# Kernel optimization log

Measured on AMD Instinct MI355X. Metric: run time of the kernel, lower is better.

Reference implementation:

```python
import jax, jax.numpy as jnp
import numpy as np
import math

B, T, D, H, L = 64, 255, 512, 8, 8
CODEBOOK = 512
V = CODEBOOK + 3  # bos/eos/pad
COND_DIM = 512
MAX_LEN = 256
HD = D // H


def _layernorm(x, g, b, eps=1e-5):
    mu = jnp.mean(x, axis=-1, keepdims=True)
    var = jnp.mean(jnp.square(x - mu), axis=-1, keepdims=True)
    return (x - mu) * jax.lax.rsqrt(var + eps) * g + b


def setup_inputs() -> dict:
    key = jax.random.key(0)
    ks = jax.random.split(key, 24)
    s = 0.02
    d = {
        'tokens': jax.random.randint(ks[0], (B, T), 0, V),
        'cond': jax.random.normal(ks[1], (B, COND_DIM), jnp.float32),
        'emb': jax.random.normal(ks[2], (V, D), jnp.float32) * s,  # tied token_emb / head weight
        'pos_emb': jax.random.normal(ks[3], (1, MAX_LEN, D), jnp.float32) * s,
        'cond_w1': jax.random.normal(ks[4], (COND_DIM, D), jnp.float32) * s,
        'cond_b1': jnp.zeros((D,), jnp.float32),
        'cond_w2': jax.random.normal(ks[5], (D, D), jnp.float32) * s,
        'cond_b2': jnp.zeros((D,), jnp.float32),
        'ln1_g': jnp.ones((L, D), jnp.float32),
        'ln1_b': jnp.zeros((L, D), jnp.float32),
        'qkv_w': jax.random.normal(ks[6], (L, D, 3 * D), jnp.float32) * s,
        'qkv_b': jnp.zeros((L, 3 * D), jnp.float32),
        'proj_w': jax.random.normal(ks[7], (L, D, D), jnp.float32) * s,
        'proj_b': jnp.zeros((L, D), jnp.float32),
        'ln2_g': jnp.ones((L, D), jnp.float32),
        'ln2_b': jnp.zeros((L, D), jnp.float32),
        'mlp_w1': jax.random.normal(ks[8], (L, D, 4 * D), jnp.float32) * s,
        'mlp_b1': jnp.zeros((L, 4 * D), jnp.float32),
        'mlp_w2': jax.random.normal(ks[9], (L, 4 * D, D), jnp.float32) * s,
        'mlp_b2': jnp.zeros((L, D), jnp.float32),
        'lnf_g': jnp.ones((D,), jnp.float32),
        'lnf_b': jnp.zeros((D,), jnp.float32),
    }
    return d


def reference(tokens, cond, emb, pos_emb, cond_w1, cond_b1, cond_w2, cond_b2,
              ln1_g, ln1_b, qkv_w, qkv_b, proj_w, proj_b,
              ln2_g, ln2_b, mlp_w1, mlp_b1, mlp_w2, mlp_b2, lnf_g, lnf_b):
    b, t = tokens.shape
    h = emb[tokens] + pos_emb[:, :t, :]                              # [B,T,D]
    c = jax.nn.silu(cond @ cond_w1 + cond_b1) @ cond_w2 + cond_b2    # [B,D]
    h = jnp.concatenate([c[:, None, :], h], axis=1)                  # [B,S,D]
    S = t + 1
    causal = jnp.tril(jnp.ones((S, S), bool))
    scale = 1.0 / math.sqrt(HD)
    for i in range(L):
        x = _layernorm(h, ln1_g[i], ln1_b[i])
        qkv = (x @ qkv_w[i] + qkv_b[i]).reshape(b, S, 3, H, HD).transpose(2, 0, 3, 1, 4)
        q, k, v = qkv[0], qkv[1], qkv[2]                             # [B,H,S,hd]
        a = jnp.einsum('bhsd,bhtd->bhst', q, k) * scale
        a = jnp.where(causal, a, -jnp.inf)
        a = jax.nn.softmax(a, axis=-1)
        o = jnp.einsum('bhst,bhtd->bhsd', a, v).transpose(0, 2, 1, 3).reshape(b, S, D)
        h = h + o @ proj_w[i] + proj_b[i]
        x = _layernorm(h, ln2_g[i], ln2_b[i])
        h = h + jax.nn.gelu(x @ mlp_w1[i] + mlp_b1[i], approximate=False) @ mlp_w2[i] + mlp_b2[i]
    h = _layernorm(h, lnf_g, lnf_b)
    return (h @ emb.T)[:, 1:, :]                                     # [B,T,V]
```

## Files before the change

kernel.cpp:

```cpp
#include <hip/hip_runtime.h>
#include <hip/hip_bf16.h>

typedef __attribute__((ext_vector_type(8))) short bf16x8;
typedef __attribute__((ext_vector_type(4))) float f32x4;
typedef __attribute__((ext_vector_type(2))) unsigned short u16x2;
typedef __attribute__((ext_vector_type(4))) unsigned short u16x4;
typedef __attribute__((ext_vector_type(8))) unsigned short u16x8;
typedef unsigned short u16;

#define DEV static __device__ __forceinline__

DEV float bf2f(u16 u) {
  union { unsigned int i; float f; } c; c.i = ((unsigned int)u) << 16; return c.f;
}
DEV u16 f2bf(float f) {
  union { float f; unsigned int i; } c; c.f = f;
  unsigned int i = c.i;
  i += 0x7FFFu + ((i >> 16) & 1u);
  return (u16)(i >> 16);
}

DEV void gload_lds16(const void* g, void* l) {
  __builtin_amdgcn_global_load_lds((const __attribute__((address_space(1))) void*)g,
                                   (__attribute__((address_space(3))) void*)l, 16, 0, 0);
}

DEV f32x4 mfma16(bf16x8 a, bf16x8 b, f32x4 c) {
  return __builtin_amdgcn_mfma_f32_16x16x32_bf16(a, b, c, 0, 0, 0);
}

template<int N> DEV void vwait() { asm volatile("s_waitcnt vmcnt(%0)" :: "n"(N) : "memory"); }

DEV float gelu(float x) {
  float t2 = __builtin_fmaf(0.044715f * x * x, x, x);
  float e = __expf(1.5957691216f * t2);
  float th = 1.f - 2.f / (e + 1.f);
  return 0.5f * x * (1.f + th);
}

__global__ __launch_bounds__(256) void ktranspose(const float* __restrict__ in, u16* __restrict__ out,
                                                  int K, int N) {
  __shared__ u16 tile[32][33];
  const float* src = in + (size_t)blockIdx.z * K * N;
  u16* dst = out + (size_t)blockIdx.z * K * N;
  const int n0 = blockIdx.x * 32, k0 = blockIdx.y * 32;
  const int tx = threadIdx.x, ty = threadIdx.y;
#pragma unroll
  for (int i = ty; i < 32; i += 8) tile[i][tx] = f2bf(src[(size_t)(k0 + i) * N + n0 + tx]);
  __syncthreads();
#pragma unroll
  for (int i = ty; i < 32; i += 8) dst[(size_t)(n0 + i) * K + k0 + tx] = tile[tx][i];
}

__global__ __launch_bounds__(256) void kcvt(const float* __restrict__ in, u16* __restrict__ out, int n) {
  int i = blockIdx.x * 256 + threadIdx.x;
  if (i < n) out[i] = f2bf(in[i]);
}

__global__ __launch_bounds__(256) void kcond(const float* __restrict__ cond, const float* __restrict__ w1,
                                             const float* __restrict__ b1, const float* __restrict__ w2,
                                             const float* __restrict__ b2, u16* __restrict__ h) {
  __shared__ float xr[512];
  __shared__ float t1[512];
  const int b = blockIdx.x, tid = threadIdx.x;
  for (int i = tid; i < 512; i += 256) xr[i] = cond[b * 512 + i];
  __syncthreads();
  for (int j = tid; j < 512; j += 256) {
    float acc = b1[j];
    for (int k = 0; k < 512; ++k) acc += xr[k] * w1[k * 512 + j];
    t1[j] = acc / (1.f + __expf(-acc));
  }
  __syncthreads();
  for (int j = tid; j < 512; j += 256) {
    float acc = b2[j];
    for (int k = 0; k < 512; ++k) acc += t1[k] * w2[k * 512 + j];
    h[(size_t)b * 256 * 512 + j] = f2bf(acc);
  }
}

__global__ __launch_bounds__(256) void kembed(const int* __restrict__ tok, const float* __restrict__ emb,
                                              const float* __restrict__ pos, u16* __restrict__ h) {
  const int idx = blockIdx.x;
  const int b = idx / 255, t = idx % 255;
  const int c = threadIdx.x * 2;
  const int tk = tok[idx];
  float2 ev = *(const float2*)(emb + (size_t)tk * 512 + c);
  float2 pv = *(const float2*)(pos + (size_t)t * 512 + c);
  u16x2 r;
  r[0] = f2bf(ev.x + pv.x);
  r[1] = f2bf(ev.y + pv.y);
  *(u16x2*)(h + ((size_t)b * 256 + 1 + t) * 512 + c) = r;
}

__global__ __launch_bounds__(256) void kln(const u16* __restrict__ hin, const float* __restrict__ g,
                                           const float* __restrict__ bt, u16* __restrict__ out) {
  const int row = blockIdx.x * 4 + (threadIdx.x >> 6), lane = threadIdx.x & 63;
  u16x8 xv = *(const u16x8*)(hin + (size_t)row * 512 + lane * 8);
  float x[8];
  float s1 = 0.f, s2 = 0.f;
#pragma unroll
  for (int j = 0; j < 8; ++j) {
    x[j] = bf2f(xv[j]);
    s1 += x[j];
    s2 += x[j] * x[j];
  }
#pragma unroll
  for (int off = 1; off < 64; off <<= 1) { s1 += __shfl_xor(s1, off); s2 += __shfl_xor(s2, off); }
  float mu = s1 * (1.f / 512.f);
  float var = s2 * (1.f / 512.f) - mu * mu;
  float rs = rsqrtf(var + 1e-5f);
  const int c0 = lane * 8;
  float4 g0 = *(const float4*)(g + c0), g1 = *(const float4*)(g + c0 + 4);
  float4 b0 = *(const float4*)(bt + c0), b1 = *(const float4*)(bt + c0 + 4);
  u16x8 o;
  o[0] = f2bf((x[0] - mu) * rs * g0.x + b0.x);
  o[1] = f2bf((x[1] - mu) * rs * g0.y + b0.y);
  o[2] = f2bf((x[2] - mu) * rs * g0.z + b0.z);
  o[3] = f2bf((x[3] - mu) * rs * g0.w + b0.w);
  o[4] = f2bf((x[4] - mu) * rs * g1.x + b1.x);
  o[5] = f2bf((x[5] - mu) * rs * g1.y + b1.y);
  o[6] = f2bf((x[6] - mu) * rs * g1.z + b1.z);
  o[7] = f2bf((x[7] - mu) * rs * g1.w + b1.w);
  *(u16x8*)(out + (size_t)row * 512 + c0) = o;
}

template<int MODE>
__global__ __launch_bounds__(256, 2) void kgemm3(const u16* __restrict__ A, const u16* __restrict__ Bt,
                                                 const float* __restrict__ bias, void* __restrict__ Cout,
                                                 int M, int N, int K) {
  __shared__ __align__(16) u16 As[3][4096];
  __shared__ __align__(16) u16 Bs[3][4096];
  const int tid = threadIdx.x;
  const int lane = tid & 63;
  const int wr = tid >> 7, wc = (tid >> 6) & 1;
  const int m0 = blockIdx.x * 128, n0 = blockIdx.y * 128;
  const int nkt = K >> 5;
  const size_t Kb = (size_t)K * 2;

  const int srow = tid >> 2;
  const int schunk = tid & 3;
  const int sc = schunk ^ ((srow >> 1) & 3);
  const int d1 = tid * 16, d2 = tid * 16 + 4096;
  int brA = n0 + srow, brB = n0 + srow + 64;
  if (MODE == 3) { brA = min(brA, N - 1); brB = min(brB, N - 1); }
  const char* Ab = (const char*)A;
  const char* Bb = (const char*)Bt;
  const size_t a0 = (size_t)(m0 + srow) * Kb + sc * 16;
  const size_t a1 = (size_t)(m0 + srow + 64) * Kb + sc * 16;
  const size_t b0 = (size_t)brA * Kb + sc * 16;
  const size_t b1 = (size_t)brB * Kb + sc * 16;

  f32x4 acc[4][4];
#pragma unroll
  for (int i = 0; i < 4; ++i)
#pragma unroll
    for (int j = 0; j < 4; ++j) acc[i][j] = f32x4{0.f, 0.f, 0.f, 0.f};

#pragma unroll
  for (int t = 0; t < 2; ++t) {
    const size_t ko = (size_t)t * 64;
    gload_lds16(Ab + a0 + ko, (char*)As[t] + d1);
    gload_lds16(Ab + a1 + ko, (char*)As[t] + d2);
    gload_lds16(Bb + b0 + ko, (char*)Bs[t] + d1);
    gload_lds16(Bb + b1 + ko, (char*)Bs[t] + d2);
  }
  asm volatile("s_waitcnt vmcnt(4)" ::: "memory");
  __builtin_amdgcn_s_barrier();
  __builtin_amdgcn_sched_barrier(0);

  const int kchunk = (((lane >> 4) ^ ((lane >> 1) & 3)) << 4);
  const int arow = wr * 64 + (lane & 15);
  const int brow = wc * 64 + (lane & 15);

  for (int kt = 0; kt < nkt; ++kt) {
    const int bufc = kt % 3;
    const bool deep = (kt + 2 < nkt);
    if (deep) {
      const int bufn = (kt + 2) % 3;
      const size_t ko = (size_t)(kt + 2) * 64;
      gload_lds16(Ab + a0 + ko, (char*)As[bufn] + d1);
      gload_lds16(Ab + a1 + ko, (char*)As[bufn] + d2);
      gload_lds16(Bb + b0 + ko, (char*)Bs[bufn] + d1);
      gload_lds16(Bb + b1 + ko, (char*)Bs[bufn] + d2);
    }
    const char* Ap = (const char*)As[bufc];
    const char* Bp = (const char*)Bs[bufc];
    bf16x8 aF[4], bF[4];
#pragma unroll
    for (int mt = 0; mt < 4; ++mt) aF[mt] = *(const bf16x8*)(Ap + (arow + mt * 16) * 64 + kchunk);
#pragma unroll
    for (int nt = 0; nt < 4; ++nt) bF[nt] = *(const bf16x8*)(Bp + (brow + nt * 16) * 64 + kchunk);
#pragma unroll
    for (int mt = 0; mt < 4; ++mt)
#pragma unroll
      for (int nt = 0; nt < 4; ++nt)
        acc[mt][nt] = mfma16(aF[mt], bF[nt], acc[mt][nt]);
    if (deep) {
      asm volatile("s_waitcnt vmcnt(4)" ::: "memory");
    } else {
      asm volatile("s_waitcnt vmcnt(0)" ::: "memory");
    }
    __builtin_amdgcn_s_barrier();
    __builtin_amdgcn_sched_barrier(0);
  }

  float bv[4];
#pragma unroll
  for (int nt = 0; nt < 4; ++nt) {
    int col = n0 + wc * 64 + nt * 16 + (lane & 15);
    bv[nt] = (MODE == 3) ? 0.f : bias[col];
  }

  if (MODE == 0 || MODE == 1) {
    u16* C = (u16*)Cout;
#pragma unroll
    for (int mt = 0; mt < 4; ++mt)
#pragma unroll
      for (int r = 0; r < 4; ++r) {
        int row = m0 + wr * 64 + mt * 16 + (lane >> 4) * 4 + r;
        u16* cp = C + (size_t)row * N + n0 + wc * 64 + (lane & 15);
#pragma unroll
        for (int nt = 0; nt < 4; ++nt) {
          float v = acc[mt][nt][r] + bv[nt];
          if (MODE == 1) v = gelu(v);
          cp[nt * 16] = f2bf(v);
        }
      }
  } else {
    float* C = (float*)Cout;
#pragma unroll
    for (int mt = 0; mt < 4; ++mt)
#pragma unroll
      for (int r = 0; r < 4; ++r) {
        int row = m0 + wr * 64 + mt * 16 + (lane >> 4) * 4 + r;
        int s = row & 255;
        if (s == 0) continue;
        int bb = row >> 8;
        float* cp = C + ((size_t)bb * 255 + (s - 1)) * 515 + n0 + wc * 64 + (lane & 15);
#pragma unroll
        for (int nt = 0; nt < 4; ++nt) {
          int col = n0 + wc * 64 + nt * 16 + (lane & 15);
          if (col < 515) cp[nt * 16] = acc[mt][nt][r];
        }
      }
  }
}

template<int FM>
__global__ __launch_bounds__(512, 2) void kgemm8(const u16* __restrict__ A, const u16* __restrict__ Bt,
                                                 const float* __restrict__ bias, u16* __restrict__ h,
                                                 int M, int N, int K) {
  constexpr int ABYTES = FM * 32 * 128;
  constexpr int BBYTES = 256 * 128;
  constexpr int AH = ABYTES / 2, BH = BBYTES / 2;
  constexpr int ALD = AH / 8192;
  constexpr int BOFF = 2 * ABYTES;
  constexpr int BM = FM * 32;
  __shared__ __align__(16) char shm[2 * ABYTES + 2 * BBYTES];

  const int tid = threadIdx.x;
  const int lane = tid & 63;
  const int wid = tid >> 6;
  const int wr = wid >> 2;
  const int wc = wid & 3;
  const int fr = lane & 15, fq = lane >> 4;
  const int axor = (fr & 7) << 4;
  const int m0 = blockIdx.x * BM, n0 = blockIdx.y * 256;
  const int nkt = K >> 6;
  const int Kb = K * 2;
  const char* Ab = (const char*)A;
  const char* Bb = (const char*)Bt;

  unsigned aOff[2][ALD], bOff[2][2];
#pragma unroll
  for (int hh = 0; hh < 2; ++hh) {
#pragma unroll
    for (int j = 0; j < ALD; ++j) {
      int d = hh * AH + j * 8192 + tid * 16;
      int row = d >> 7, pc = (d >> 4) & 7;
      aOff[hh][j] = (unsigned)((m0 + row) * Kb + ((pc ^ (row & 7)) << 4));
    }
#pragma unroll
    for (int j = 0; j < 2; ++j) {
      int d = hh * BH + j * 8192 + tid * 16;
      int row = d >> 7, pc = (d >> 4) & 7;
      bOff[hh][j] = (unsigned)((n0 + row) * Kb + ((pc ^ (row & 7)) << 4));
    }
  }

  auto stA = [&](int kt, int hh, int b) {
#pragma unroll
    for (int j = 0; j < ALD; ++j)
      gload_lds16(Ab + (size_t)aOff[hh][j] + (size_t)kt * 128,
                  shm + b * ABYTES + hh * AH + j * 8192 + tid * 16);
  };
  auto stB = [&](int kt, int hh, int b) {
#pragma unroll
    for (int j = 0; j < 2; ++j)
      gload_lds16(Bb + (size_t)bOff[hh][j] + (size_t)kt * 128,
                  shm + BOFF + b * BBYTES + hh * BH + j * 8192 + tid * 16);
  };
  auto rdA = [&](int b, int m, int ks) {
    return *(const bf16x8*)(shm + b * ABYTES + (wr * (BM / 2) + m * 16 + fr) * 128 +
                            ((ks * 64 + fq * 16) ^ axor));
  };
  auto rdB = [&](int b, int n, int ks) {
    return *(const bf16x8*)(shm + BOFF + b * BBYTES + (wc * 64 + n * 16 + fr) * 128 +
                            ((ks * 64 + fq * 16) ^ axor));
  };

  f32x4 acc[FM][4];
#pragma unroll
  for (int i = 0; i < FM; ++i)
#pragma unroll
    for (int j = 0; j < 4; ++j) acc[i][j] = f32x4{0.f, 0.f, 0.f, 0.f};

  stA(0, 0, 0); stA(0, 1, 0); stB(0, 0, 0); stB(0, 1, 0);
  if (nkt > 1) { stA(1, 0, 1); stA(1, 1, 1); }
  vwait<2 * ALD>();
  __builtin_amdgcn_sched_barrier(0);
  __builtin_amdgcn_s_barrier();

  for (int kt = 0; kt < nkt; ++kt) {
    const int cur = kt & 1;
    const bool sb = (kt + 1 < nkt);
    const bool sa = (kt + 2 < nkt);
    bf16x8 aF[FM][2], bF[4][2];
#pragma unroll
    for (int m = 0; m < FM; ++m) aF[m][0] = rdA(cur, m, 0);
#pragma unroll
    for (int n = 0; n < 4; ++n) bF[n][0] = rdB(cur, n, 0);
    if (sb) stB(kt + 1, 0, cur ^ 1);
    __builtin_amdgcn_s_barrier();
    __builtin_amdgcn_s_setprio(1);
#pragma unroll
    for (int m = 0; m < FM / 2; ++m)
#pragma unroll
      for (int n = 0; n < 4; ++n) acc[m][n] = mfma16(aF[m][0], bF[n][0], acc[m][n]);
    __builtin_amdgcn_s_setprio(0);
    __builtin_amdgcn_s_barrier();
#pragma unroll
    for (int m = 0; m < FM; ++m) aF[m][1] = rdA(cur, m, 1);
#pragma unroll
    for (int n = 0; n < 4; ++n) bF[n][1] = rdB(cur, n, 1);
    if (sb) stB(kt + 1, 1, cur ^ 1);
    __builtin_amdgcn_s_barrier();
    __builtin_amdgcn_s_setprio(1);
#pragma unroll
    for (int m = FM / 2; m < FM; ++m)
#pragma unroll
      for (int n = 0; n < 4; ++n) acc[m][n] = mfma16(aF[m][0], bF[n][0], acc[m][n]);
    __builtin_amdgcn_s_setprio(0);
    asm volatile("s_waitcnt lgkmcnt(0)" ::: "memory");
    __builtin_amdgcn_sched_barrier(0);
    __builtin_amdgcn_s_barrier();
    if (sa) stA(kt + 2, 0, cur);
    __builtin_amdgcn_s_barrier();
    __builtin_amdgcn_s_setprio(1);
#pragma unroll
    for (int m = 0; m < FM / 2; ++m)
#pragma unroll
      for (int n = 0; n < 4; ++n) acc[m][n] = mfma16(aF[m][1], bF[n][1], acc[m][n]);
    __builtin_amdgcn_s_setprio(0);
    __builtin_amdgcn_s_barrier();
    if (sa) stA(kt + 2, 1, cur);
    __builtin_amdgcn_s_barrier();
    __builtin_amdgcn_s_setprio(1);
#pragma unroll
    for (int m = FM / 2; m < FM; ++m)
#pragma unroll
      for (int n = 0; n < 4; ++n) acc[m][n] = mfma16(aF[m][1], bF[n][1], acc[m][n]);
    __builtin_amdgcn_s_setprio(0);
    if (sa) vwait<2 * ALD>(); else vwait<0>();
    __builtin_amdgcn_sched_barrier(0);
    __builtin_amdgcn_s_barrier();
  }

  float bv[4];
#pragma unroll
  for (int n = 0; n < 4; ++n) bv[n] = bias[n0 + wc * 64 + n * 16 + fr];

#pragma unroll
  for (int m = 0; m < FM; ++m)
#pragma unroll
    for (int r = 0; r < 4; ++r) {
      int row = m0 + wr * (BM / 2) + m * 16 + fq * 4 + r;
      u16* hp = h + (size_t)row * N + n0 + wc * 64 + fr;
#pragma unroll
      for (int n = 0; n < 4; ++n) {
        float val = acc[m][n][r] + bv[n] + bf2f(hp[n * 16]);
        hp[n * 16] = f2bf(val);
      }
    }
}

__global__ __launch_bounds__(256, 1) void kattn(const u16* __restrict__ qkv, u16* __restrict__ o) {
  __shared__ __align__(16) u16 Ks[256][72];
  __shared__ __align__(16) u16 Vt[64][264];
  __shared__ __align__(16) u16 Ps[4][64][72];
  const int tid = threadIdx.x, wv = tid >> 6, lane = tid & 63;
  const int bh = blockIdx.x, bb = bh >> 3, hh = bh & 7;
  const size_t base = (size_t)bb * 256 * 1536 + hh * 64;

  for (int c = tid; c < 2048; c += 256) {
    int s = c >> 3, pp = c & 7;
    u16x8 kv = *(const u16x8*)(qkv + base + (size_t)s * 1536 + 512 + pp * 8);
    *(u16x8*)&Ks[s][pp * 8] = kv;
    u16x8 vv = *(const u16x8*)(qkv + base + (size_t)s * 1536 + 1024 + pp * 8);
#pragma unroll
    for (int j = 0; j < 8; ++j) Vt[pp * 8 + j][s] = vv[j];
  }
  __syncthreads();

  bf16x8 qf[4][2];
#pragma unroll
  for (int mt = 0; mt < 4; ++mt)
#pragma unroll
    for (int ks = 0; ks < 2; ++ks)
      qf[mt][ks] = *(const bf16x8*)(qkv + base +
                   (size_t)(wv * 64 + mt * 16 + (lane & 15)) * 1536 + ks * 32 + (lane >> 4) * 8);

  const float scale = 0.125f;
  float mrow[4][4], lsum[4][4];
#pragma unroll
  for (int mt = 0; mt < 4; ++mt)
#pragma unroll
    for (int r = 0; r < 4; ++r) { mrow[mt][r] = -1e30f; lsum[mt][r] = 0.f; }

  f32x4 oacc[4][4];
#pragma unroll
  for (int i = 0; i < 4; ++i)
#pragma unroll
    for (int j = 0; j < 4; ++j) oacc[i][j] = f32x4{0.f, 0.f, 0.f, 0.f};

  for (int ct = 0; ct <= wv; ++ct) {
    f32x4 sacc[4][4];
#pragma unroll
    for (int i = 0; i < 4; ++i)
#pragma unroll
      for (int j = 0; j < 4; ++j) sacc[i][j] = f32x4{0.f, 0.f, 0.f, 0.f};
#pragma unroll
    for (int ks = 0; ks < 2; ++ks) {
      bf16x8 kf[4];
#pragma unroll
      for (int nt = 0; nt < 4; ++nt)
        kf[nt] = *(const bf16x8*)&Ks[ct * 64 + nt * 16 + (lane & 15)][ks * 32 + (lane >> 4) * 8];
#pragma unroll
      for (int mt = 0; mt < 4; ++mt)
#pragma unroll
        for (int nt = 0; nt < 4; ++nt)
          sacc[mt][nt] = mfma16(qf[mt][ks], kf[nt], sacc[mt][nt]);
    }
#pragma unroll
    for (int mt = 0; mt < 4; ++mt)
#pragma unroll
      for (int r = 0; r < 4; ++r) {
        int srow = wv * 64 + mt * 16 + (lane >> 4) * 4 + r;
        float v[4];
        float mx = -1e30f;
#pragma unroll
        for (int nt = 0; nt < 4; ++nt) {
          int tcol = ct * 64 + nt * 16 + (lane & 15);
          float vv = sacc[mt][nt][r] * scale;
          v[nt] = (tcol > srow) ? -1e30f : vv;
          mx = fmaxf(mx, v[nt]);
        }
#pragma unroll
        for (int off = 1; off < 16; off <<= 1) mx = fmaxf(mx, __shfl_xor(mx, off));
        float mnew = fmaxf(mrow[mt][r], mx);
        float sf = __expf(mrow[mt][r] - mnew);
        mrow[mt][r] = mnew;
        float ps = 0.f;
#pragma unroll
        for (int nt = 0; nt < 4; ++nt) {
          float pe = (v[nt] <= -1e29f) ? 0.f : __expf(v[nt] - mnew);
          ps += pe;
          Ps[wv][mt * 16 + (lane >> 4) * 4 + r][nt * 16 + (lane & 15)] = f2bf(pe);
        }
#pragma unroll
        for (int off = 1; off < 16; off <<= 1) ps += __shfl_xor(ps, off);
        lsum[mt][r] = lsum[mt][r] * sf + ps;
#pragma unroll
        for (int nt = 0; nt < 4; ++nt) oacc[mt][nt][r] *= sf;
      }
#pragma unroll
    for (int ks = 0; ks < 2; ++ks) {
      bf16x8 pf[4], vf[4];
#pragma unroll
      for (int mt = 0; mt < 4; ++mt)
        pf[mt] = *(const bf16x8*)&Ps[wv][mt * 16 + (lane & 15)][ks * 32 + (lane >> 4) * 8];
#pragma unroll
      for (int nt = 0; nt < 4; ++nt)
        vf[nt] = *(const bf16x8*)&Vt[nt * 16 + (lane & 15)][ct * 64 + ks * 32 + (lane >> 4) * 8];
#pragma unroll
      for (int mt = 0; mt < 4; ++mt)
#pragma unroll
        for (int nt = 0; nt < 4; ++nt)
          oacc[mt][nt] = mfma16(pf[mt], vf[nt], oacc[mt][nt]);
    }
  }

#pragma unroll
  for (int mt = 0; mt < 4; ++mt)
#pragma unroll
    for (int r = 0; r < 4; ++r) {
      int s = wv * 64 + mt * 16 + (lane >> 4) * 4 + r;
      float inv = 1.f / lsum[mt][r];
      u16* op = o + ((size_t)bb * 256 + s) * 512 + hh * 64 + (lane & 15);
#pragma unroll
      for (int nt = 0; nt < 4; ++nt) op[nt * 16] = f2bf(oacc[mt][nt][r] * inv);
    }
}

extern "C" void kernel_launch(void* const* d_in, const int* in_sizes, int n_in,
                              void* d_out, int out_size, void* d_ws, size_t ws_size,
                              hipStream_t stream) {
  const int* tokens = (const int*)d_in[0];
  const float* cond = (const float*)d_in[1];
  const float* emb = (const float*)d_in[2];
  const float* pos = (const float*)d_in[3];
  const float* cw1 = (const float*)d_in[4];
  const float* cb1 = (const float*)d_in[5];
  const float* cw2 = (const float*)d_in[6];
  const float* cb2 = (const float*)d_in[7];
  const float* ln1g = (const float*)d_in[8];
  const float* ln1b = (const float*)d_in[9];
  const float* qkvw = (const float*)d_in[10];
  const float* qkvb = (const float*)d_in[11];
  const float* projw = (const float*)d_in[12];
  const float* projb = (const float*)d_in[13];
  const float* ln2g = (const float*)d_in[14];
  const float* ln2b = (const float*)d_in[15];
  const float* w1 = (const float*)d_in[16];
  const float* b1 = (const float*)d_in[17];
  const float* w2 = (const float*)d_in[18];
  const float* b2 = (const float*)d_in[19];
  const float* lnfg = (const float*)d_in[20];
  const float* lnfb = (const float*)d_in[21];

  const size_t NEEDED = (size_t)16384 * 512 * 2
                      + (size_t)16384 * 512 * 2
                      + (size_t)16384 * 2048 * 2
                      + (size_t)8 * 1536 * 512 * 2
                      + (size_t)8 * 512 * 512 * 2
                      + (size_t)8 * 2048 * 512 * 2
                      + (size_t)8 * 512 * 2048 * 2;
  if (ws_size < NEEDED) return;

  char* p = (char*)d_ws;
  u16* h = (u16*)p;            p += (size_t)16384 * 512 * 2;
  u16* xln = (u16*)p;          p += (size_t)16384 * 512 * 2;
  u16* big = (u16*)p;          p += (size_t)16384 * 2048 * 2;
  u16* attn_o = big + (size_t)16384 * 1536;
  u16* embB = big;
  u16* qkvT = (u16*)p;         p += (size_t)8 * 1536 * 512 * 2;
  u16* projT = (u16*)p;        p += (size_t)8 * 512 * 512 * 2;
  u16* w1T = (u16*)p;          p += (size_t)8 * 2048 * 512 * 2;
  u16* w2T = (u16*)p;          p += (size_t)8 * 512 * 2048 * 2;

  ktranspose<<<dim3(48, 16, 8), dim3(32, 8), 0, stream>>>(qkvw, qkvT, 512, 1536);
  ktranspose<<<dim3(16, 16, 8), dim3(32, 8), 0, stream>>>(projw, projT, 512, 512);
  ktranspose<<<dim3(64, 16, 8), dim3(32, 8), 0, stream>>>(w1, w1T, 512, 2048);
  ktranspose<<<dim3(16, 64, 8), dim3(32, 8), 0, stream>>>(w2, w2T, 2048, 512);

  kembed<<<16320, 256, 0, stream>>>(tokens, emb, pos, h);
  kcond<<<64, 256, 0, stream>>>(cond, cw1, cb1, cw2, cb2, h);

  for (int l = 0; l < 8; ++l) {
    kln<<<4096, 256, 0, stream>>>(h, ln1g + l * 512, ln1b + l * 512, xln);
    kgemm3<0><<<dim3(128, 12), 256, 0, stream>>>(xln, qkvT + (size_t)l * 1536 * 512,
                                                 qkvb + l * 1536, big, 16384, 1536, 512);
    kattn<<<512, 256, 0, stream>>>(big, attn_o);
    kgemm8<4><<<dim3(128, 2), 512, 0, stream>>>(attn_o, projT + (size_t)l * 512 * 512,
                                                projb + l * 512, h, 16384, 512, 512);
    kln<<<4096, 256, 0, stream>>>(h, ln2g + l * 512, ln2b + l * 512, xln);
    kgemm3<1><<<dim3(128, 16), 256, 0, stream>>>(xln, w1T + (size_t)l * 2048 * 512,
                                                 b1 + l * 2048, big, 16384, 2048, 512);
    kgemm8<4><<<dim3(128, 2), 512, 0, stream>>>(big, w2T + (size_t)l * 512 * 2048,
                                                b2 + l * 512, h, 16384, 512, 2048);
  }
  kln<<<4096, 256, 0, stream>>>(h, lnfg, lnfb, xln);
  kcvt<<<1030, 256, 0, stream>>>(emb, embB, 515 * 512);
  kgemm3<3><<<dim3(128, 5), 256, 0, stream>>>(xln, embB, nullptr, d_out, 16384, 515, 512);
}
```

Baseline: 1.878 ms.

## Keep full-K weight panel resident in LDS for QKV and MLP-up GEMMs

Adds a GEMM kernel that loads a 128xK weight panel into shared memory once per block and streams eight 128-row A tiles through a triple-buffered pipeline. The bias and GELU epilogue is written out after each M tile. QKV and MLP-up projections switch to it. This avoids reloading the weight tile for every M tile, but it uses about 128 KB of LDS for one block per CU, a much smaller grid, and serialised epilogues inside the main loop.

```diff
diff --git a/kernel.cpp b/kernel.cpp
--- a/kernel.cpp
+++ b/kernel.cpp
@@ -124,6 +124,106 @@
   *(u16x8*)(out + (size_t)row * 512 + c0) = o;
 }
 
+template<int MODE, int MT>
+__global__ __launch_bounds__(256, 1) void kgemmbs(const u16* __restrict__ A, const u16* __restrict__ Bt,
+                                                  const float* __restrict__ bias, u16* __restrict__ C,
+                                                  int M, int N, int K) {
+  __shared__ __align__(16) u16 Bp[128 * 512];
+  __shared__ __align__(16) u16 As[3][4096];
+  const int tid = threadIdx.x, lane = tid & 63;
+  const int wr = tid >> 7, wc = (tid >> 6) & 1;
+  const int fr = lane & 15, fq = lane >> 4;
+  const int n0 = blockIdx.y * 128;
+  const int m0 = blockIdx.x * (MT * 128);
+  const int NKT = 16;
+  const size_t Kb = (size_t)K * 2;
+  const char* Ab = (const char*)A;
+  const char* Bb = (const char*)Bt;
+
+#pragma unroll
+  for (int j = 0; j < 32; ++j) {
+    int d = tid * 16 + j * 4096;
+    int row = d >> 10, off = d & 1023;
+    gload_lds16(Bb + (size_t)(n0 + row) * Kb + (off ^ ((row & 7) << 4)), (char*)Bp + d);
+  }
+
+  const int srow = tid >> 2;
+  const int sc = (tid & 3) ^ ((srow >> 1) & 3);
+  const int d1 = tid * 16, d2 = tid * 16 + 4096;
+  auto stageA = [&](int g, int buf) {
+    const int mt = g >> 4, kt = g & 15;
+    const size_t base = (size_t)(m0 + mt * 128 + srow) * Kb + kt * 64 + sc * 16;
+    gload_lds16(Ab + base, (char*)As[buf] + d1);
+    gload_lds16(Ab + base + (size_t)64 * Kb, (char*)As[buf] + d2);
+  };
+
+  stageA(0, 0);
+  stageA(1, 1);
+  asm volatile("s_waitcnt vmcnt(2)" ::: "memory");
+  __builtin_amdgcn_s_barrier();
+  __builtin_amdgcn_sched_barrier(0);
+
+  const int kchunkA = (((lane >> 4) ^ ((lane >> 1) & 3)) << 4);
+  const int arow = wr * 64 + fr;
+  const int brow0 = wc * 64 + fr;
+
+  f32x4 acc[4][4];
+#pragma unroll
+  for (int i = 0; i < 4; ++i)
+#pragma unroll
+    for (int j = 0; j < 4; ++j) acc[i][j] = f32x4{0.f, 0.f, 0.f, 0.f};
+
+  float bv[4], dummy = 0.f;
+#pragma unroll
+  for (int nt = 0; nt < 4; ++nt) bv[nt] = bias[n0 + wc * 64 + nt * 16 + fr];
+
+  const int TOT = MT * NKT;
+  for (int g = 0; g < TOT; ++g) {
+    const int kt = g & 15;
+    const int bufc = g % 3;
+    if (g + 2 < TOT) stageA(g + 2, (g + 2) % 3);
+    const char* Ap = (const char*)As[bufc];
+    bf16x8 aF[4], bF[4];
+#pragma unroll
+    for (int mt4 = 0; mt4 < 4; ++mt4)
+      aF[mt4] = *(const bf16x8*)(Ap + (arow + mt4 * 16) * 64 + kchunkA);
+#pragma unroll
+    for (int nt = 0; nt < 4; ++nt) {
+      const int nrow = brow0 + nt * 16;
+      const int koff = (kt * 64 + fq * 16) ^ ((nrow & 7) << 4);
+      bF[nt] = *(const bf16x8*)((const char*)Bp + nrow * 1024 + koff);
+    }
+#pragma unroll
+    for (int mt4 = 0; mt4 < 4; ++mt4)
+#pragma unroll
+      for (int nt = 0; nt < 4; ++nt)
+        acc[mt4][nt] = mfma16(aF[mt4], bF[nt], acc[mt4][nt]);
+
+    if (kt == 15) {
+      const int mt = g >> 4;
+      u16* Cb = C + (size_t)(m0 + mt * 128) * N + n0;
+#pragma unroll
+      for (int mm = 0; mm < 4; ++mm)
+#pragma unroll
+        for (int r = 0; r < 4; ++r) {
+          int row = mm * 16 + wr * 64 + fq * 4 + r;
+          u16* cp = Cb + (size_t)row * N + wc * 64 + fr;
+#pragma unroll
+          for (int nt = 0; nt < 4; ++nt) {
+            float v = acc[mm][nt][r] + bv[nt];
+            if (MODE == 1) v = gelu(v);
+            cp[nt * 16] = f2bf(v);
+            acc[mm][nt][r] = 0.f;
+          }
+        }
+    }
+    if (g + 2 < TOT) vwait<2>(); else vwait<0>();
+    __builtin_amdgcn_s_barrier();
+    __builtin_amdgcn_sched_barrier(0);
+  }
+  (void)dummy;
+}
+
 template<int MODE>
 __global__ __launch_bounds__(256, 2) void kgemm3(const u16* __restrict__ A, const u16* __restrict__ Bt,
                                                  const float* __restrict__ bias, void* __restrict__ Cout,
@@ -138,8 +238,7 @@
   const size_t Kb = (size_t)K * 2;
 
   const int srow = tid >> 2;
-  const int schunk = tid & 3;
-  const int sc = schunk ^ ((srow >> 1) & 3);
+  const int sc = (tid & 3) ^ ((srow >> 1) & 3);
   const int d1 = tid * 16, d2 = tid * 16 + 4096;
   int brA = n0 + srow, brB = n0 + srow + 64;
   if (MODE == 3) { brA = min(brA, N - 1); brB = min(brB, N - 1); }
@@ -204,46 +303,22 @@
     __builtin_amdgcn_sched_barrier(0);
   }
 
-  float bv[4];
-#pragma unroll
-  for (int nt = 0; nt < 4; ++nt) {
-    int col = n0 + wc * 64 + nt * 16 + (lane & 15);
-    bv[nt] = (MODE == 3) ? 0.f : bias[col];
-  }
-
-  if (MODE == 0 || MODE == 1) {
-    u16* C = (u16*)Cout;
-#pragma unroll
-    for (int mt = 0; mt < 4; ++mt)
-#pragma unroll
-      for (int r = 0; r < 4; ++r) {
-        int row = m0 + wr * 64 + mt * 16 + (lane >> 4) * 4 + r;
-        u16* cp = C + (size_t)row * N + n0 + wc * 64 + (lane & 15);
-#pragma unroll
-        for (int nt = 0; nt < 4; ++nt) {
-          float v = acc[mt][nt][r] + bv[nt];
-          if (MODE == 1) v = gelu(v);
-          cp[nt * 16] = f2bf(v);
-        }
+  float* Cf = (float*)Cout;
+#pragma unroll
+  for (int mt = 0; mt < 4; ++mt)
+#pragma unroll
+    for (int r = 0; r < 4; ++r) {
+      int row = m0 + wr * 64 + mt * 16 + (lane >> 4) * 4 + r;
+      int s = row & 255;
+      if (s == 0) continue;
+      int bb = row >> 8;
+      float* cp = Cf + ((size_t)bb * 255 + (s - 1)) * 515 + n0 + wc * 64 + (lane & 15);
+#pragma unroll
+      for (int nt = 0; nt < 4; ++nt) {
+        int col = n0 + wc * 64 + nt * 16 + (lane & 15);
+        if (col < 515) cp[nt * 16] = acc[mt][nt][r];
       }
-  } else {
-    float* C = (float*)Cout;
-#pragma unroll
-    for (int mt = 0; mt < 4; ++mt)
-#pragma unroll
-      for (int r = 0; r < 4; ++r) {
-        int row = m0 + wr * 64 + mt * 16 + (lane >> 4) * 4 + r;
-        int s = row & 255;
-        if (s == 0) continue;
-        int bb = row >> 8;
-        float* cp = C + ((size_t)bb * 255 + (s - 1)) * 515 + n0 + wc * 64 + (lane & 15);
-#pragma unroll
-        for (int nt = 0; nt < 4; ++nt) {
-          int col = n0 + wc * 64 + nt * 16 + (lane & 15);
-          if (col < 515) cp[nt * 16] = acc[mt][nt][r];
-        }
-      }
-  }
+    }
 }
 
 template<int FM>
@@ -568,14 +643,14 @@
 
   for (int l = 0; l < 8; ++l) {
     kln<<<4096, 256, 0, stream>>>(h, ln1g + l * 512, ln1b + l * 512, xln);
-    kgemm3<0><<<dim3(128, 12), 256, 0, stream>>>(xln, qkvT + (size_t)l * 1536 * 512,
-                                                 qkvb + l * 1536, big, 16384, 1536, 512);
+    kgemmbs<0, 8><<<dim3(16, 12), 256, 0, stream>>>(xln, qkvT + (size_t)l * 1536 * 512,
+                                                    qkvb + l * 1536, big, 16384, 1536, 512);
     kattn<<<512, 256, 0, stream>>>(big, attn_o);
     kgemm8<4><<<dim3(128, 2), 512, 0, stream>>>(attn_o, projT + (size_t)l * 512 * 512,
                                                 projb + l * 512, h, 16384, 512, 512);
     kln<<<4096, 256, 0, stream>>>(h, ln2g + l * 512, ln2b + l * 512, xln);
-    kgemm3<1><<<dim3(128, 16), 256, 0, stream>>>(xln, w1T + (size_t)l * 2048 * 512,
-                                                 b1 + l * 2048, big, 16384, 2048, 512);
+    kgemmbs<1, 8><<<dim3(16, 16), 256, 0, stream>>>(xln, w1T + (size_t)l * 2048 * 512,
+                                                    b1 + l * 2048, big, 16384, 2048, 512);
     kgemm8<4><<<dim3(128, 2), 512, 0, stream>>>(big, w2T + (size_t)l * 512 * 2048,
                                                 b2 + l * 512, h, 16384, 512, 2048);
   }
```

After: 3.085 ms, median of 2. 64.3% more time.
